# Performance work log

Hardware: AMD Instinct MI355X
Metric: run time of the kernel (lower is better)

## Reference

```python
import jax, jax.numpy as jnp
import numpy as np

B, S, H, E, I = 2, 2048, 1024, 8, 4096
NUM_SELECT = 2


def setup_inputs() -> dict:
    key = jax.random.key(0)
    ks = jax.random.split(key, 6)
    scale = 0.02
    x = jax.random.normal(ks[0], (B, S, H), dtype=jnp.float32)
    Wg = jax.random.normal(ks[1], (H, E), dtype=jnp.float32) * scale
    W1 = jax.random.normal(ks[2], (E, H, I), dtype=jnp.float32) * scale
    b1 = jnp.zeros((E, I), dtype=jnp.float32)
    W2 = jax.random.normal(ks[3], (E, I, H), dtype=jnp.float32) * scale
    b2 = jnp.zeros((E, H), dtype=jnp.float32)
    return {"x": x, "Wg": Wg, "W1": W1, "b1": b1, "W2": W2, "b2": b2}


def reference(x, Wg, W1, b1, W2, b2):
    b, s, h = x.shape
    e = Wg.shape[1]
    xf = x.reshape(-1, h)                       # [T, H], T = b*s
    T = xf.shape[0]

    logits = xf @ Wg                            # [T, E]
    probs = jax.nn.softmax(logits, axis=-1)
    topk_p, topk_i = jax.lax.top_k(probs, NUM_SELECT)   # [T, k]
    topk_p = topk_p / topk_p.sum(axis=-1, keepdims=True)

    # combine weight per (token, expert): w[t, e] = sum_k topk_p[t, k] * 1[topk_i[t, k] == e]
    # top_k indices within a row are distinct, so scatter-add is exact.
    w = jnp.zeros((T, e), dtype=xf.dtype).at[jnp.arange(T)[:, None], topk_i].add(topk_p)

    # Dense per-expert FFN, weighted combine (weight is 0 for unrouted tokens,
    # so math matches the masked gather/scatter loop of the original).
    out = jnp.zeros_like(xf)
    for ei in range(e):  # small fixed loop over experts
        hdn = jax.nn.silu(xf @ W1[ei] + b1[ei])          # [T, I]
        y = hdn @ W2[ei] + b2[ei]                        # [T, H]
        out = out + w[:, ei:ei + 1] * y
    return out.reshape(b, s, h)
```

## Files before the change

### kernel.cpp

```cpp
#include <hip/hip_runtime.h>
#include <cstdint>
#include <cstddef>

using u16 = unsigned short;
typedef __bf16 bf16x8 __attribute__((ext_vector_type(8)));
typedef float f32x4 __attribute__((ext_vector_type(4)));
typedef u16 u16x8 __attribute__((ext_vector_type(8)));

#define T_TOK 4096
#define HDIM 1024
#define EXP 8
#define IDIM 4096
#define NROWS 8192
#define PAD_ROWS 8320
#define BM 128
#define BN 128
#define BK 64
#define MAX_TILES 72

__device__ __forceinline__ u16 f2bf(float f) {
  union { float f; uint32_t u; } v; v.f = f;
  uint32_t u = v.u;
  u += 0x7fffu + ((u >> 16) & 1u);
  return (u16)(u >> 16);
}

__device__ __forceinline__ void async_copy16(const u16* g, u16* s) {
  __builtin_amdgcn_global_load_lds((__attribute__((address_space(1))) void*)(void*)g,
                                   (__attribute__((address_space(3))) void*)s, 16, 0, 0);
}

__global__ __launch_bounds__(256) void gate_kernel(const float* __restrict__ x,
                                                   const float* __restrict__ Wg,
                                                   int* __restrict__ sel_e,
                                                   float* __restrict__ sel_w) {
  int lane = threadIdx.x & 63;
  int wave = threadIdx.x >> 6;
  int t = blockIdx.x * 4 + wave;
  const float* xr = x + (size_t)t * HDIM;
  float p[8];
#pragma unroll
  for (int e = 0; e < 8; ++e) p[e] = 0.f;
#pragma unroll
  for (int i = 0; i < 16; ++i) {
    int h = i * 64 + lane;
    float xv = xr[h];
    const float4* w4 = (const float4*)(Wg + h * 8);
    float4 a = w4[0], b = w4[1];
    p[0] += xv * a.x; p[1] += xv * a.y; p[2] += xv * a.z; p[3] += xv * a.w;
    p[4] += xv * b.x; p[5] += xv * b.y; p[6] += xv * b.z; p[7] += xv * b.w;
  }
#pragma unroll
  for (int e = 0; e < 8; ++e) {
#pragma unroll
    for (int off = 32; off > 0; off >>= 1) p[e] += __shfl_xor(p[e], off);
  }
  if (lane == 0) {
    int e0 = 0; float m0 = p[0];
#pragma unroll
    for (int e = 1; e < 8; ++e) { if (p[e] > m0) { m0 = p[e]; e0 = e; } }
    int e1 = -1; float m1 = -3.4e38f;
#pragma unroll
    for (int e = 0; e < 8; ++e) { if (e != e0 && p[e] > m1) { m1 = p[e]; e1 = e; } }
    float r = expf(m1 - m0);
    float w0 = 1.f / (1.f + r);
    float w1 = r / (1.f + r);
    sel_e[2 * t] = e0; sel_e[2 * t + 1] = e1;
    sel_w[2 * t] = w0; sel_w[2 * t + 1] = w1;
  }
}

__global__ void route_kernel(const int* __restrict__ sel_e, const float* __restrict__ sel_w,
                             int* __restrict__ row_token, float* __restrict__ row_weight,
                             int* __restrict__ tile_e, int* __restrict__ tile_m0,
                             int* __restrict__ tile_nrows, int* __restrict__ num_tiles) {
  __shared__ int cnt[EXP], off[EXP], cur[EXP];
  int tid = threadIdx.x;
  if (tid < EXP) { cnt[tid] = 0; cur[tid] = 0; }
  __syncthreads();
  for (int i = tid; i < NROWS; i += 256) atomicAdd(&cnt[sel_e[i]], 1);
  __syncthreads();
  if (tid == 0) {
    int running = 0, nt = 0;
    for (int e = 0; e < EXP; ++e) {
      off[e] = running;
      int c = cnt[e];
      int ntile = (c + BM - 1) / BM;
      for (int j = 0; j < ntile; ++j) {
        tile_e[nt] = e;
        tile_m0[nt] = running + j * BM;
        tile_nrows[nt] = min(BM, c - j * BM);
        ++nt;
      }
      running += c;
    }
    *num_tiles = nt;
  }
  __syncthreads();
  for (int i = tid; i < NROWS; i += 256) {
    int e = sel_e[i];
    int pos = off[e] + atomicAdd(&cur[e], 1);
    row_token[pos] = i >> 1;
    row_weight[pos] = sel_w[i];
  }
}

__global__ __launch_bounds__(256) void gather_kernel(const float* __restrict__ x,
                                                     const int* __restrict__ row_token,
                                                     u16* __restrict__ xg) {
  int r = blockIdx.x;
  int tok = row_token[r];
  const float4* xs = (const float4*)(x + (size_t)tok * HDIM);
  float4 v = xs[threadIdx.x];
  ushort4 o;
  o.x = f2bf(v.x); o.y = f2bf(v.y); o.z = f2bf(v.z); o.w = f2bf(v.w);
  *(ushort4*)(xg + (size_t)r * HDIM + threadIdx.x * 4) = o;
}

__global__ __launch_bounds__(256) void transpose_convert(const float* __restrict__ src,
                                                         u16* __restrict__ dst, int R, int C) {
  int eb = blockIdx.z;
  const float* s = src + (size_t)eb * R * C;
  u16* d = dst + (size_t)eb * R * C;
  int cb = blockIdx.x * 64, rb = blockIdx.y * 64;
  __shared__ u16 tile[64][65];
  int tid = threadIdx.x;
#pragma unroll
  for (int i = 0; i < 4; ++i) {
    int idx = i * 256 + tid;
    int r = idx >> 4;
    int c4 = (idx & 15) * 4;
    float4 v = *(const float4*)(s + (size_t)(rb + r) * C + cb + c4);
    tile[r][c4]     = f2bf(v.x);
    tile[r][c4 + 1] = f2bf(v.y);
    tile[r][c4 + 2] = f2bf(v.z);
    tile[r][c4 + 3] = f2bf(v.w);
  }
  __syncthreads();
#pragma unroll
  for (int i = 0; i < 2; ++i) {
    int idx = i * 256 + tid;
    int c = idx >> 3;
    int r8 = (idx & 7) * 8;
    u16x8 o;
#pragma unroll
    for (int j = 0; j < 8; ++j) o[j] = tile[r8 + j][c];
    *(u16x8*)(d + (size_t)(cb + c) * R + rb + r8) = o;
  }
}

template <int K, bool SECOND>
__global__ __launch_bounds__(256, 2) void ffn_gemm(
    const u16* __restrict__ A, const u16* __restrict__ B,
    const float* __restrict__ bias, u16* __restrict__ hdn_out,
    float* __restrict__ out, const int* __restrict__ row_token,
    const float* __restrict__ row_weight, const int* __restrict__ tile_e,
    const int* __restrict__ tile_m0, const int* __restrict__ tile_nrows,
    const int* __restrict__ num_tiles, int N, int kchunk) {
  int ty = blockIdx.y;
  if (ty >= *num_tiles) return;
  int e = tile_e[ty];
  int row0 = tile_m0[ty];
  int nrows = tile_nrows[ty];
  int n0 = blockIdx.x * BN;
  int kz = blockIdx.z;
  int kbase = kz * kchunk;

  __shared__ u16 sA[BM * BK];
  __shared__ u16 sB[BN * BK];

  int tid = threadIdx.x;
  int lane = tid & 63;
  int wave = tid >> 6;
  int wm = wave >> 1, wn = wave & 1;
  int l15 = lane & 15, quad = lane >> 4;
  int r7 = l15 & 7;

  const u16* Ab = A + (size_t)row0 * K;
  const u16* Bb = B + (size_t)e * (size_t)N * K + (size_t)n0 * K;

  const u16* pA[4]; const u16* pB[4];
  u16* dA[4]; u16* dB[4];
#pragma unroll
  for (int i = 0; i < 4; ++i) {
    int c = i * 256 + tid;
    int row = c >> 3;
    int j = (c & 7) ^ (row & 7);
    pA[i] = Ab + (size_t)row * K + j * 8 + kbase;
    pB[i] = Bb + (size_t)row * K + j * 8 + kbase;
    dA[i] = sA + c * 8;
    dB[i] = sB + c * 8;
  }

  int abase[4], bbase[4];
#pragma unroll
  for (int i = 0; i < 4; ++i) {
    abase[i] = (wm * 64 + i * 16 + l15) * BK;
    bbase[i] = (wn * 64 + i * 16 + l15) * BK;
  }
  int jx[2];
#pragma unroll
  for (int ks = 0; ks < 2; ++ks) jx[ks] = ((ks * 4 + quad) ^ r7) * 8;

  f32x4 acc[4][4];
#pragma unroll
  for (int am = 0; am < 4; ++am)
#pragma unroll
    for (int an = 0; an < 4; ++an) acc[am][an] = (f32x4){0.f, 0.f, 0.f, 0.f};

  for (int k0 = 0; k0 < kchunk; k0 += BK) {
#pragma unroll
    for (int i = 0; i < 4; ++i) {
      async_copy16(pA[i] + k0, dA[i]);
      async_copy16(pB[i] + k0, dB[i]);
    }
    __syncthreads();
#pragma unroll
    for (int ks = 0; ks < 2; ++ks) {
      bf16x8 af[4], bfr[4];
#pragma unroll
      for (int i = 0; i < 4; ++i) af[i] = *(const bf16x8*)(sA + abase[i] + jx[ks]);
#pragma unroll
      for (int i = 0; i < 4; ++i) bfr[i] = *(const bf16x8*)(sB + bbase[i] + jx[ks]);
#pragma unroll
      for (int am = 0; am < 4; ++am)
#pragma unroll
        for (int an = 0; an < 4; ++an)
          acc[am][an] = __builtin_amdgcn_mfma_f32_16x16x32_bf16(af[am], bfr[an],
                                                               acc[am][an], 0, 0, 0);
    }
    __syncthreads();
  }

  if (!SECOND) {
#pragma unroll
    for (int an = 0; an < 4; ++an) {
      int col = n0 + wn * 64 + an * 16 + l15;
      float bv = bias[e * N + col];
#pragma unroll
      for (int am = 0; am < 4; ++am) {
#pragma unroll
        for (int r = 0; r < 4; ++r) {
          int lr = wm * 64 + am * 16 + quad * 4 + r;
          if (lr < nrows) {
            float vv = acc[am][an][r] + bv;
            vv = vv / (1.f + __expf(-vv));
            hdn_out[(size_t)(row0 + lr) * N + col] = f2bf(vv);
          }
        }
      }
    }
  } else {
    float bv[4];
#pragma unroll
    for (int an = 0; an < 4; ++an)
      bv[an] = (kz == 0) ? bias[e * N + n0 + wn * 64 + an * 16 + l15] : 0.f;
#pragma unroll
    for (int am = 0; am < 4; ++am) {
#pragma unroll
      for (int r = 0; r < 4; ++r) {
        int lr = wm * 64 + am * 16 + quad * 4 + r;
        if (lr < nrows) {
          int grow = row0 + lr;
          int tok = row_token[grow];
          float w = row_weight[grow];
          float* orow = out + (size_t)tok * N;
#pragma unroll
          for (int an = 0; an < 4; ++an) {
            int col = n0 + wn * 64 + an * 16 + l15;
            atomicAdd(orow + col, (acc[am][an][r] + bv[an]) * w);
          }
        }
      }
    }
  }
}

extern "C" void kernel_launch(void* const* d_in, const int* in_sizes, int n_in,
                              void* d_out, int out_size, void* d_ws, size_t ws_size,
                              hipStream_t stream) {
  const float* x  = (const float*)d_in[0];
  const float* Wg = (const float*)d_in[1];
  const float* W1 = (const float*)d_in[2];
  const float* b1 = (const float*)d_in[3];
  const float* W2 = (const float*)d_in[4];
  const float* b2 = (const float*)d_in[5];
  float* out = (float*)d_out;

  char* ws = (char*)d_ws;
  size_t off = 0;
  auto alloc = [&](size_t bytes) {
    void* p = ws + off;
    off += (bytes + 255) & ~(size_t)255;
    return p;
  };
  u16* W1T = (u16*)alloc((size_t)EXP * IDIM * HDIM * 2);
  u16* W2T = (u16*)alloc((size_t)EXP * IDIM * HDIM * 2);
  u16* xg  = (u16*)alloc((size_t)PAD_ROWS * HDIM * 2);
  u16* hdn = (u16*)alloc((size_t)PAD_ROWS * IDIM * 2);
  int*   sel_e      = (int*)alloc(NROWS * 4);
  float* sel_w      = (float*)alloc(NROWS * 4);
  int*   row_token  = (int*)alloc(NROWS * 4);
  float* row_weight = (float*)alloc(NROWS * 4);
  int* tile_e     = (int*)alloc(MAX_TILES * 4);
  int* tile_m0    = (int*)alloc(MAX_TILES * 4);
  int* tile_nrows = (int*)alloc(MAX_TILES * 4);
  int* num_tiles  = (int*)alloc(4);

  hipMemsetAsync(d_out, 0, (size_t)out_size * sizeof(float), stream);
  transpose_convert<<<dim3(IDIM / 64, HDIM / 64, EXP), 256, 0, stream>>>(W1, W1T, HDIM, IDIM);
  transpose_convert<<<dim3(HDIM / 64, IDIM / 64, EXP), 256, 0, stream>>>(W2, W2T, IDIM, HDIM);
  gate_kernel<<<T_TOK / 4, 256, 0, stream>>>(x, Wg, sel_e, sel_w);
  route_kernel<<<1, 256, 0, stream>>>(sel_e, sel_w, row_token, row_weight,
                                      tile_e, tile_m0, tile_nrows, num_tiles);
  gather_kernel<<<NROWS, 256, 0, stream>>>(x, row_token, xg);
  ffn_gemm<HDIM, false><<<dim3(IDIM / BN, MAX_TILES, 1), 256, 0, stream>>>(
      xg, W1T, b1, hdn, nullptr, nullptr, nullptr,
      tile_e, tile_m0, tile_nrows, num_tiles, IDIM, HDIM);
  ffn_gemm<IDIM, true><<<dim3(HDIM / BN, MAX_TILES, 2), 256, 0, stream>>>(
      hdn, W2T, b2, nullptr, out, row_token, row_weight,
      tile_e, tile_m0, tile_nrows, num_tiles, HDIM, IDIM / 2);
}
```

Measured before the change: 622.9 us.

## Replace atomic scatter-add with bf16 partial buffers and a gather combine kernel

The second GEMM now writes each split-K partial result as bf16 into a per-split buffer instead of doing fp32 atomicAdd into the output. A new combine kernel uses an inverse row map to gather each token's two expert rows from both splits, applies the routing weights and writes the output directly, which also removes the output memset. The grid is transposed so tiles vary fastest, and launch bounds are raised to allow three blocks per SM. This removes atomic contention but adds an extra kernel and the bf16 rounding of partial sums, which lowers accuracy.

New measurement: 630.9 us. No clear change (+1.3%).

```diff
diff --git a/kernel.cpp b/kernel.cpp
--- a/kernel.cpp
+++ b/kernel.cpp
@@ -25,6 +25,10 @@
   return (u16)(u >> 16);
 }
 
+__device__ __forceinline__ float bf2f(u16 u) {
+  union { uint32_t i; float f; } v; v.i = (uint32_t)u << 16; return v.f;
+}
+
 __device__ __forceinline__ void async_copy16(const u16* g, u16* s) {
   __builtin_amdgcn_global_load_lds((__attribute__((address_space(1))) void*)(void*)g,
                                    (__attribute__((address_space(3))) void*)s, 16, 0, 0);
@@ -71,7 +75,7 @@
 }
 
 __global__ void route_kernel(const int* __restrict__ sel_e, const float* __restrict__ sel_w,
-                             int* __restrict__ row_token, float* __restrict__ row_weight,
+                             int* __restrict__ row_token, int* __restrict__ inv_row,
                              int* __restrict__ tile_e, int* __restrict__ tile_m0,
                              int* __restrict__ tile_nrows, int* __restrict__ num_tiles) {
   __shared__ int cnt[EXP], off[EXP], cur[EXP];
@@ -101,7 +105,7 @@
     int e = sel_e[i];
     int pos = off[e] + atomicAdd(&cur[e], 1);
     row_token[pos] = i >> 1;
-    row_weight[pos] = sel_w[i];
+    inv_row[i] = pos;
   }
 }
 
@@ -150,19 +154,18 @@
 }
 
 template <int K, bool SECOND>
-__global__ __launch_bounds__(256, 2) void ffn_gemm(
+__global__ __launch_bounds__(256, 3) void ffn_gemm(
     const u16* __restrict__ A, const u16* __restrict__ B,
-    const float* __restrict__ bias, u16* __restrict__ hdn_out,
-    float* __restrict__ out, const int* __restrict__ row_token,
-    const float* __restrict__ row_weight, const int* __restrict__ tile_e,
+    const float* __restrict__ bias, u16* __restrict__ ybuf,
+    const int* __restrict__ tile_e,
     const int* __restrict__ tile_m0, const int* __restrict__ tile_nrows,
     const int* __restrict__ num_tiles, int N, int kchunk) {
-  int ty = blockIdx.y;
+  int ty = blockIdx.x;
   if (ty >= *num_tiles) return;
   int e = tile_e[ty];
   int row0 = tile_m0[ty];
   int nrows = tile_nrows[ty];
-  int n0 = blockIdx.x * BN;
+  int n0 = blockIdx.y * BN;
   int kz = blockIdx.z;
   int kbase = kz * kchunk;
 
@@ -232,48 +235,44 @@
     __syncthreads();
   }
 
-  if (!SECOND) {
-#pragma unroll
-    for (int an = 0; an < 4; ++an) {
-      int col = n0 + wn * 64 + an * 16 + l15;
-      float bv = bias[e * N + col];
-#pragma unroll
-      for (int am = 0; am < 4; ++am) {
-#pragma unroll
-        for (int r = 0; r < 4; ++r) {
-          int lr = wm * 64 + am * 16 + quad * 4 + r;
-          if (lr < nrows) {
-            float vv = acc[am][an][r] + bv;
-            vv = vv / (1.f + __expf(-vv));
-            hdn_out[(size_t)(row0 + lr) * N + col] = f2bf(vv);
-          }
+  u16* dstbase = ybuf + (size_t)kz * PAD_ROWS * N;
+#pragma unroll
+  for (int an = 0; an < 4; ++an) {
+    int col = n0 + wn * 64 + an * 16 + l15;
+    float bv = (kz == 0) ? bias[e * N + col] : 0.f;
+#pragma unroll
+    for (int am = 0; am < 4; ++am) {
+#pragma unroll
+      for (int r = 0; r < 4; ++r) {
+        int lr = wm * 64 + am * 16 + quad * 4 + r;
+        if (lr < nrows) {
+          float vv = acc[am][an][r] + bv;
+          if (!SECOND) vv = vv / (1.f + __expf(-vv));
+          dstbase[(size_t)(row0 + lr) * N + col] = f2bf(vv);
         }
       }
     }
-  } else {
-    float bv[4];
-#pragma unroll
-    for (int an = 0; an < 4; ++an)
-      bv[an] = (kz == 0) ? bias[e * N + n0 + wn * 64 + an * 16 + l15] : 0.f;
-#pragma unroll
-    for (int am = 0; am < 4; ++am) {
-#pragma unroll
-      for (int r = 0; r < 4; ++r) {
-        int lr = wm * 64 + am * 16 + quad * 4 + r;
-        if (lr < nrows) {
-          int grow = row0 + lr;
-          int tok = row_token[grow];
-          float w = row_weight[grow];
-          float* orow = out + (size_t)tok * N;
-#pragma unroll
-          for (int an = 0; an < 4; ++an) {
-            int col = n0 + wn * 64 + an * 16 + l15;
-            atomicAdd(orow + col, (acc[am][an][r] + bv[an]) * w);
-          }
-        }
-      }
-    }
-  }
+  }
+}
+
+__global__ __launch_bounds__(256) void combine_kernel(const u16* __restrict__ y,
+                                                      const int* __restrict__ inv_row,
+                                                      const float* __restrict__ sel_w,
+                                                      float* __restrict__ out) {
+  int t = blockIdx.x;
+  int c = threadIdx.x * 4;
+  int r0 = inv_row[2 * t], r1 = inv_row[2 * t + 1];
+  float w0 = sel_w[2 * t], w1 = sel_w[2 * t + 1];
+  ushort4 a0 = *(const ushort4*)(y + ((size_t)0 * PAD_ROWS + r0) * HDIM + c);
+  ushort4 a1 = *(const ushort4*)(y + ((size_t)1 * PAD_ROWS + r0) * HDIM + c);
+  ushort4 b0 = *(const ushort4*)(y + ((size_t)0 * PAD_ROWS + r1) * HDIM + c);
+  ushort4 b1 = *(const ushort4*)(y + ((size_t)1 * PAD_ROWS + r1) * HDIM + c);
+  float4 o;
+  o.x = w0 * (bf2f(a0.x) + bf2f(a1.x)) + w1 * (bf2f(b0.x) + bf2f(b1.x));
+  o.y = w0 * (bf2f(a0.y) + bf2f(a1.y)) + w1 * (bf2f(b0.y) + bf2f(b1.y));
+  o.z = w0 * (bf2f(a0.z) + bf2f(a1.z)) + w1 * (bf2f(b0.z) + bf2f(b1.z));
+  o.w = w0 * (bf2f(a0.w) + bf2f(a1.w)) + w1 * (bf2f(b0.w) + bf2f(b1.w));
+  *(float4*)(out + (size_t)t * HDIM + c) = o;
 }
 
 extern "C" void kernel_launch(void* const* d_in, const int* in_sizes, int n_in,
@@ -298,26 +297,25 @@
   u16* W2T = (u16*)alloc((size_t)EXP * IDIM * HDIM * 2);
   u16* xg  = (u16*)alloc((size_t)PAD_ROWS * HDIM * 2);
   u16* hdn = (u16*)alloc((size_t)PAD_ROWS * IDIM * 2);
+  u16* y   = (u16*)alloc((size_t)2 * PAD_ROWS * HDIM * 2);
   int*   sel_e      = (int*)alloc(NROWS * 4);
   float* sel_w      = (float*)alloc(NROWS * 4);
   int*   row_token  = (int*)alloc(NROWS * 4);
-  float* row_weight = (float*)alloc(NROWS * 4);
+  int*   inv_row    = (int*)alloc(NROWS * 4);
   int* tile_e     = (int*)alloc(MAX_TILES * 4);
   int* tile_m0    = (int*)alloc(MAX_TILES * 4);
   int* tile_nrows = (int*)alloc(MAX_TILES * 4);
   int* num_tiles  = (int*)alloc(4);
 
-  hipMemsetAsync(d_out, 0, (size_t)out_size * sizeof(float), stream);
   transpose_convert<<<dim3(IDIM / 64, HDIM / 64, EXP), 256, 0, stream>>>(W1, W1T, HDIM, IDIM);
   transpose_convert<<<dim3(HDIM / 64, IDIM / 64, EXP), 256, 0, stream>>>(W2, W2T, IDIM, HDIM);
   gate_kernel<<<T_TOK / 4, 256, 0, stream>>>(x, Wg, sel_e, sel_w);
-  route_kernel<<<1, 256, 0, stream>>>(sel_e, sel_w, row_token, row_weight,
+  route_kernel<<<1, 256, 0, stream>>>(sel_e, sel_w, row_token, inv_row,
                                       tile_e, tile_m0, tile_nrows, num_tiles);
   gather_kernel<<<NROWS, 256, 0, stream>>>(x, row_token, xg);
-  ffn_gemm<HDIM, false><<<dim3(IDIM / BN, MAX_TILES, 1), 256, 0, stream>>>(
-      xg, W1T, b1, hdn, nullptr, nullptr, nullptr,
-      tile_e, tile_m0, tile_nrows, num_tiles, IDIM, HDIM);
-  ffn_gemm<IDIM, true><<<dim3(HDIM / BN, MAX_TILES, 2), 256, 0, stream>>>(
-      hdn, W2T, b2, nullptr, out, row_token, row_weight,
-      tile_e, tile_m0, tile_nrows, num_tiles, HDIM, IDIM / 2);
-}
+  ffn_gemm<HDIM, false><<<dim3(MAX_TILES, IDIM / BN, 1), 256, 0, stream>>>(
+      xg, W1T, b1, hdn, tile_e, tile_m0, tile_nrows, num_tiles, IDIM, HDIM);
+  ffn_gemm<IDIM, true><<<dim3(MAX_TILES, HDIM / BN, 2), 256, 0, stream>>>(
+      hdn, W2T, b2, y, tile_e, tile_m0, tile_nrows, num_tiles, HDIM, IDIM / 2);
+  combine_kernel<<<T_TOK, 256, 0, stream>>>(y, inv_row, sel_w, out);
+}
```
